# Kernel optimization log

Measured on AMD Instinct MI355X. Metric: run time of the kernel, lower is better.

The kernel has to match this reference:

```python
import jax, jax.numpy as jnp
import numpy as np

N_NODES = 50000
N_EDGES = 800000
IN_DIM = 128
HID = 128
N_GRAPHS = 256
N_CLASSES = 2
ALPHA = 0.2  # leaky relu slope
EPS_BN = 1e-5


def setup_inputs() -> dict:
    key = jax.random.key(0)
    ks = jax.random.split(key, 24)
    adjacency = jax.random.randint(ks[0], (2, N_EDGES), 0, N_NODES, dtype=jnp.int32)
    input_feature = jax.random.normal(ks[1], (N_NODES, IN_DIM), dtype=jnp.float32)
    graph_indicator = jnp.sort(jax.random.randint(ks[2], (N_NODES,), 0, N_GRAPHS, dtype=jnp.int32))
    labels = jax.random.randint(ks[3], (N_GRAPHS,), 0, N_CLASSES, dtype=jnp.int64)
    s = 0.05
    params = {
        'W1': jax.random.normal(ks[4], (IN_DIM, HID), jnp.float32) * s,
        'a1': jax.random.normal(ks[5], (2 * HID,), jnp.float32) * s,
        'bn2_g': jnp.ones((HID,), jnp.float32),
        'bn2_b': jnp.zeros((HID,), jnp.float32),
        'W2': jax.random.normal(ks[6], (HID, HID), jnp.float32) * s,
        'a2': jax.random.normal(ks[7], (2 * HID,), jnp.float32) * s,
        'bn3_g': jnp.ones((HID,), jnp.float32),
        'bn3_b': jnp.zeros((HID,), jnp.float32),
        'W3': jax.random.normal(ks[8], (HID, HID), jnp.float32) * s,
        'a3': jax.random.normal(ks[9], (2 * HID,), jnp.float32) * s,
        'fc1_w': jax.random.normal(ks[10], (HID, 2 * HID), jnp.float32) * s,
        'fc1_b': jnp.zeros((2 * HID,), jnp.float32),
        'fc2_w': jax.random.normal(ks[11], (2 * HID, HID), jnp.float32) * s,
        'fc2_b': jnp.zeros((HID,), jnp.float32),
        'fc3_w': jax.random.normal(ks[12], (HID, N_CLASSES), jnp.float32) * s,
        'fc3_b': jnp.zeros((N_CLASSES,), jnp.float32),
    }
    return dict(adjacency=adjacency, input_feature=input_feature,
                graph_indicator=graph_indicator, labels=labels, **params)


def _batchnorm(x, g, b):
    # training-mode BatchNorm1d over node dim (biased variance)
    mu = jnp.mean(x, axis=0)
    var = jnp.mean((x - mu) ** 2, axis=0)
    return (x - mu) * jax.lax.rsqrt(var + EPS_BN) * g + b


def _sp_gat(x, src, dst, W, a):
    # pyGAT SpGraphAttentionLayer (dropout disabled / eval mode)
    h = x @ W                                # [N, F]
    F = h.shape[1]
    e_src = h @ a[:F]                        # [N]
    e_dst = h @ a[F:]                        # [N]
    e = e_src[src] + e_dst[dst]              # [E]
    ee = jnp.exp(-jax.nn.leaky_relu(e, ALPHA))
    rowsum = jax.ops.segment_sum(ee, src, num_segments=N_NODES)          # [N]
    num = jax.ops.segment_sum(ee[:, None] * h[dst], src, num_segments=N_NODES)  # [N, F]
    h_prime = num / (rowsum[:, None] + 1e-16)
    return jax.nn.elu(h_prime)


def reference(adjacency, input_feature, graph_indicator, labels,
              W1, a1, bn2_g, bn2_b, W2, a2, bn3_g, bn3_b, W3, a3,
              fc1_w, fc1_b, fc2_w, fc2_b, fc3_w, fc3_b):
    src, dst = adjacency[0], adjacency[1]
    # bn1 output is discarded in the original forward
    x = _sp_gat(input_feature, src, dst, W1, a1)
    x = _batchnorm(x, bn2_g, bn2_b)
    x = _sp_gat(x, src, dst, W2, a2)
    x = _batchnorm(x, bn3_g, bn3_b)
    x = _sp_gat(x, src, dst, W3, a3)
    # pooling_sum_4tensor: per-graph sum pooling
    pooled = jax.ops.segment_sum(x, graph_indicator, num_segments=N_GRAPHS)  # [G, F]
    x = jax.nn.relu(pooled @ fc1_w + fc1_b)
    x = jax.nn.relu(x @ fc2_w + fc2_b)
    logits = x @ fc3_w + fc3_b
    return logits
```

## Files before the change

kernel.cpp:

```cpp
#include <hip/hip_runtime.h>
#include <hip/hip_bf16.h>

#define N_NODES 50000
#define N_EDGES 800000
#define FD 128
#define N_GRAPHS 256
#define NPART 6250

typedef unsigned short u16;
typedef short bf16x8 __attribute__((ext_vector_type(8)));
typedef float f32x4 __attribute__((ext_vector_type(4)));

__device__ __forceinline__ u16 f2bf(float v) {
    __hip_bfloat16 h = __float2bfloat16(v);
    union { __hip_bfloat16 hh; u16 u; } c; c.hh = h; return c.u;
}
__device__ __forceinline__ float bf2f(u16 r) {
    return __uint_as_float(((unsigned int)r) << 16);
}

__global__ __launch_bounds__(256) void count_deg_part_k(const int* __restrict__ src,
                                                        int* __restrict__ cnt, int E) {
    int part = blockIdx.x & 7;
    int lo = part * NPART, hi = lo + NPART;
    int stride = (gridDim.x >> 3) * 256;
    for (int e = (blockIdx.x >> 3) * 256 + threadIdx.x; e < E; e += stride) {
        int s = src[e];
        if (s >= lo && s < hi) atomicAdd(&cnt[s], 1);
    }
}

__global__ __launch_bounds__(256) void fill_csr_part_k(const int* __restrict__ src,
                                                       const int* __restrict__ dst,
                                                       int* __restrict__ cur,
                                                       int* __restrict__ edst, int E) {
    int part = blockIdx.x & 7;
    int lo = part * NPART, hi = lo + NPART;
    int stride = (gridDim.x >> 3) * 256;
    for (int e = (blockIdx.x >> 3) * 256 + threadIdx.x; e < E; e += stride) {
        int s = src[e];
        if (s >= lo && s < hi) {
            int p = atomicAdd(&cur[s], 1);
            edst[p] = dst[e];
        }
    }
}

__global__ __launch_bounds__(256) void scan1_k(const int* __restrict__ cnt,
                                               int* __restrict__ bsum, int M,
                                               float* __restrict__ bnbuf,
                                               float* __restrict__ pooled) {
    int i = blockIdx.x * 256 + threadIdx.x;
    int v = (i < M) ? cnt[i] : 0;
    __shared__ int l[256];
    l[threadIdx.x] = v;
    __syncthreads();
    for (int s = 128; s > 0; s >>= 1) {
        if (threadIdx.x < s) l[threadIdx.x] += l[threadIdx.x + s];
        __syncthreads();
    }
    if (threadIdx.x == 0) bsum[blockIdx.x] = l[0];
    if (blockIdx.x == 0) {
        bnbuf[threadIdx.x] = 0.f; bnbuf[threadIdx.x + 256] = 0.f;
        for (int k = threadIdx.x; k < N_GRAPHS * FD; k += 256) pooled[k] = 0.f;
    }
}

__global__ __launch_bounds__(256) void scan3_k(const int* __restrict__ cnt,
                                               const int* __restrict__ bsum,
                                               int* __restrict__ offs,
                                               int* __restrict__ cur, int M, int NB) {
    int i = blockIdx.x * 256 + threadIdx.x;
    int tid = threadIdx.x;
    __shared__ int bs[256];
    bs[tid] = (tid < NB) ? bsum[tid] : 0;
    __syncthreads();
    for (int off = 1; off < 256; off <<= 1) {
        int t = (tid >= off) ? bs[tid - off] : 0;
        __syncthreads();
        bs[tid] += t;
        __syncthreads();
    }
    int base = (blockIdx.x == 0) ? 0 : bs[blockIdx.x - 1];
    int v = (i < M) ? cnt[i] : 0;
    __shared__ int l[256];
    l[tid] = v;
    __syncthreads();
    for (int off = 1; off < 256; off <<= 1) {
        int t = (tid >= off) ? l[tid - off] : 0;
        __syncthreads();
        l[tid] += t;
        __syncthreads();
    }
    int excl = l[tid] - v + base;
    if (i < M) { offs[i] = excl; cur[i] = excl; }
    if (i == M - 1) offs[M] = excl + v;
}

__global__ __launch_bounds__(256) void gemm_mfma_k(const float* __restrict__ Xf,
                                                   const u16* __restrict__ Xb,
                                                   int use_f32,
                                                   const float* __restrict__ W,
                                                   const float* __restrict__ sums,
                                                   const float* __restrict__ sumsq,
                                                   const float* __restrict__ g,
                                                   const float* __restrict__ b,
                                                   float invN, int haveBN,
                                                   const float* __restrict__ avec,
                                                   u16* __restrict__ Hb,
                                                   float* __restrict__ es,
                                                   float* __restrict__ ed, int M) {
    __shared__ u16 As[64][136];
    __shared__ u16 Bs[128][136];
    __shared__ float cv[128];
    __shared__ float scsh[256];
    int tid = threadIdx.x;
    int row0 = blockIdx.x * 64;

    if (haveBN) {
        if (tid < 128) {
            float mu = sums[tid] * invN;
            float var = sumsq[tid] * invN - mu * mu;
            float sc = g[tid] * rsqrtf(var + 1e-5f);
            scsh[tid] = sc;
            scsh[128 + tid] = b[tid] - mu * sc;
        }
        __syncthreads();
        float cvp = 0.f;
#pragma unroll 8
        for (int i = 0; i < 64; i++) {
            int idx = i * 256 + tid;
            int k = idx >> 7;
            int n = idx & 127;
            float wv = W[idx];
            Bs[n][k] = f2bf(scsh[k] * wv);
            cvp += scsh[128 + k] * wv;
        }
        __syncthreads();
        scsh[tid] = cvp;
        __syncthreads();
        if (tid < 128) cv[tid] = scsh[tid] + scsh[tid + 128];
    } else {
#pragma unroll 8
        for (int i = 0; i < 64; i++) {
            int idx = i * 256 + tid;
            Bs[idx & 127][idx >> 7] = f2bf(W[idx]);
        }
        if (tid < 128) cv[tid] = 0.f;
    }

    {
        int r = tid >> 2, k0 = (tid & 3) * 32;
        int grow = row0 + r;
        if (grow < M) {
            if (use_f32) {
                const float4* s = (const float4*)(Xf + (size_t)grow * FD + k0);
#pragma unroll
                for (int u = 0; u < 8; u++) {
                    float4 v = s[u];
                    ushort4 o;
                    o.x = f2bf(v.x); o.y = f2bf(v.y); o.z = f2bf(v.z); o.w = f2bf(v.w);
                    *(ushort4*)&As[r][k0 + u * 4] = o;
                }
            } else {
                const uint4* s = (const uint4*)(Xb + (size_t)grow * FD + k0);
#pragma unroll
                for (int u = 0; u < 4; u++) *(uint4*)&As[r][k0 + u * 8] = s[u];
            }
        } else {
            uint4 z = make_uint4(0, 0, 0, 0);
#pragma unroll
            for (int u = 0; u < 4; u++) *(uint4*)&As[r][k0 + u * 8] = z;
        }
    }
    __syncthreads();

    int wave = tid >> 6, lane = tid & 63;
    int quad = lane >> 4, n16 = lane & 15;
    int rbase = wave * 16;
    f32x4 acc[8];
    f32x4 zz = {0.f, 0.f, 0.f, 0.f};
#pragma unroll
    for (int t = 0; t < 8; t++) acc[t] = zz;

#pragma unroll
    for (int kk = 0; kk < 128; kk += 32) {
        bf16x8 a = *(const bf16x8*)&As[rbase + n16][kk + quad * 8];
#pragma unroll
        for (int t = 0; t < 8; t++) {
            bf16x8 bb = *(const bf16x8*)&Bs[t * 16 + n16][kk + quad * 8];
            acc[t] = __builtin_amdgcn_mfma_f32_16x16x32_bf16(a, bb, acc[t], 0, 0, 0);
        }
    }

    float sas[8], sad[8];
#pragma unroll
    for (int t = 0; t < 8; t++) {
        sas[t] = avec[t * 16 + n16];
        sad[t] = avec[128 + t * 16 + n16];
    }

#pragma unroll
    for (int reg = 0; reg < 4; reg++) {
        int grow = row0 + rbase + quad * 4 + reg;
        float vals[8];
        float ps = 0.f, pd = 0.f;
#pragma unroll
        for (int t = 0; t < 8; t++) {
            float v = acc[t][reg] + cv[t * 16 + n16];
            vals[t] = v;
            ps += v * sas[t];
            pd += v * sad[t];
        }
#pragma unroll
        for (int o = 8; o > 0; o >>= 1) { ps += __shfl_xor(ps, o); pd += __shfl_xor(pd, o); }
        if (grow < M) {
            if (n16 == 0) { es[grow] = ps; ed[grow] = pd; }
#pragma unroll
            for (int t = 0; t < 8; t++)
                Hb[(size_t)grow * FD + t * 16 + n16] = f2bf(vals[t]);
        }
    }
}

__global__ __launch_bounds__(256) void agg_k(const u16* __restrict__ Hb,
                                             const float* __restrict__ es_,
                                             const float* __restrict__ ed_,
                                             const int* __restrict__ offs,
                                             const int* __restrict__ edst,
                                             u16* __restrict__ Out, int M) {
    int node = __builtin_amdgcn_readfirstlane((int)((blockIdx.x * blockDim.x + threadIdx.x) >> 6));
    int lane = threadIdx.x & 63;
    if (node >= M) return;
    int s0 = offs[node], s1 = offs[node + 1];
    float esv = es_[node];
    const unsigned int* Hrow = (const unsigned int*)Hb;
    float2 a0 = make_float2(0.f, 0.f), a1 = make_float2(0.f, 0.f);
    float2 a2 = make_float2(0.f, 0.f), a3 = make_float2(0.f, 0.f);
    float rs = 0.f;
    int e = s0;
    for (; e + 8 <= s1; e += 8) {
        int d0 = __builtin_amdgcn_readfirstlane(edst[e]);
        int d1 = __builtin_amdgcn_readfirstlane(edst[e + 1]);
        int d2 = __builtin_amdgcn_readfirstlane(edst[e + 2]);
        int d3 = __builtin_amdgcn_readfirstlane(edst[e + 3]);
        int d4 = __builtin_amdgcn_readfirstlane(edst[e + 4]);
        int d5 = __builtin_amdgcn_readfirstlane(edst[e + 5]);
        int d6 = __builtin_amdgcn_readfirstlane(edst[e + 6]);
        int d7 = __builtin_amdgcn_readfirstlane(edst[e + 7]);
        float w0, w1, w2, w3, w4, w5, w6, w7;
        {
            float ev = esv + ed_[d0]; float lr = ev > 0.f ? ev : 0.2f * ev; w0 = __expf(-lr);
        }
        { float ev = esv + ed_[d1]; float lr = ev > 0.f ? ev : 0.2f * ev; w1 = __expf(-lr); }
        { float ev = esv + ed_[d2]; float lr = ev > 0.f ? ev : 0.2f * ev; w2 = __expf(-lr); }
        { float ev = esv + ed_[d3]; float lr = ev > 0.f ? ev : 0.2f * ev; w3 = __expf(-lr); }
        { float ev = esv + ed_[d4]; float lr = ev > 0.f ? ev : 0.2f * ev; w4 = __expf(-lr); }
        { float ev = esv + ed_[d5]; float lr = ev > 0.f ? ev : 0.2f * ev; w5 = __expf(-lr); }
        { float ev = esv + ed_[d6]; float lr = ev > 0.f ? ev : 0.2f * ev; w6 = __expf(-lr); }
        { float ev = esv + ed_[d7]; float lr = ev > 0.f ? ev : 0.2f * ev; w7 = __expf(-lr); }
        unsigned int r0 = Hrow[(size_t)d0 * 64 + lane];
        unsigned int r1 = Hrow[(size_t)d1 * 64 + lane];
        unsigned int r2 = Hrow[(size_t)d2 * 64 + lane];
        unsigned int r3 = Hrow[(size_t)d3 * 64 + lane];
        unsigned int r4 = Hrow[(size_t)d4 * 64 + lane];
        unsigned int r5 = Hrow[(size_t)d5 * 64 + lane];
        unsigned int r6 = Hrow[(size_t)d6 * 64 + lane];
        unsigned int r7 = Hrow[(size_t)d7 * 64 + lane];
        rs += w0 + w1 + w2 + w3 + w4 + w5 + w6 + w7;
        a0.x += w0 * __uint_as_float(r0 << 16);
        a0.y += w0 * __uint_as_float(r0 & 0xffff0000u);
        a1.x += w1 * __uint_as_float(r1 << 16);
        a1.y += w1 * __uint_as_float(r1 & 0xffff0000u);
        a2.x += w2 * __uint_as_float(r2 << 16);
        a2.y += w2 * __uint_as_float(r2 & 0xffff0000u);
        a3.x += w3 * __uint_as_float(r3 << 16);
        a3.y += w3 * __uint_as_float(r3 & 0xffff0000u);
        a0.x += w4 * __uint_as_float(r4 << 16);
        a0.y += w4 * __uint_as_float(r4 & 0xffff0000u);
        a1.x += w5 * __uint_as_float(r5 << 16);
        a1.y += w5 * __uint_as_float(r5 & 0xffff0000u);
        a2.x += w6 * __uint_as_float(r6 << 16);
        a2.y += w6 * __uint_as_float(r6 & 0xffff0000u);
        a3.x += w7 * __uint_as_float(r7 << 16);
        a3.y += w7 * __uint_as_float(r7 & 0xffff0000u);
    }
    for (; e < s1; e++) {
        int d = __builtin_amdgcn_readfirstlane(edst[e]);
        float ev = esv + ed_[d];
        float lr = ev > 0.f ? ev : 0.2f * ev;
        float wv = __expf(-lr);
        rs += wv;
        unsigned int r = Hrow[(size_t)d * 64 + lane];
        a0.x += wv * __uint_as_float(r << 16);
        a0.y += wv * __uint_as_float(r & 0xffff0000u);
    }
    float inv = 1.f / (rs + 1e-16f);
    float vx = (a0.x + a1.x + a2.x + a3.x) * inv;
    float vy = (a0.y + a1.y + a2.y + a3.y) * inv;
    vx = vx > 0.f ? vx : (__expf(vx) - 1.f);
    vy = vy > 0.f ? vy : (__expf(vy) - 1.f);
    unsigned int pk = ((unsigned int)f2bf(vy) << 16) | f2bf(vx);
    ((unsigned int*)Out)[(size_t)node * 64 + lane] = pk;
}

__global__ void bnstats_b_k(const u16* __restrict__ Xb, float* __restrict__ sums,
                            float* __restrict__ sumsq, int M) {
    int f = threadIdx.x & 127;
    int half = threadIdx.x >> 7;
    float s1 = 0.f, s2 = 0.f;
    for (int r = blockIdx.x * 2 + half; r < M; r += gridDim.x * 2) {
        float v = bf2f(Xb[(size_t)r * FD + f]);
        s1 += v; s2 += v * v;
    }
    __shared__ float l1[256], l2[256];
    l1[threadIdx.x] = s1; l2[threadIdx.x] = s2;
    __syncthreads();
    if (half == 0) {
        atomicAdd(&sums[f], l1[f] + l1[f + 128]);
        atomicAdd(&sumsq[f], l2[f] + l2[f + 128]);
    }
}

__global__ void pool_k(const u16* __restrict__ Xb, const int* __restrict__ gi,
                       float* __restrict__ pooled, int M) {
    int f = threadIdx.x & 127;
    int half = threadIdx.x >> 7;
    int r0 = blockIdx.x * 128 + half;
    int rend = min(blockIdx.x * 128 + 128, M);
    int curg = -1; float acc = 0.f;
    for (int r = r0; r < rend; r += 2) {
        int g = gi[r];
        if (g != curg) {
            if (curg >= 0) atomicAdd(&pooled[(size_t)curg * FD + f], acc);
            curg = g; acc = 0.f;
        }
        acc += bf2f(Xb[(size_t)r * FD + f]);
    }
    if (curg >= 0) atomicAdd(&pooled[(size_t)curg * FD + f], acc);
}

__global__ __launch_bounds__(256) void mlp_k(const float* __restrict__ pooled,
                                             const float* __restrict__ fc1w, const float* __restrict__ fc1b,
                                             const float* __restrict__ fc2w, const float* __restrict__ fc2b,
                                             const float* __restrict__ fc3w, const float* __restrict__ fc3b,
                                             float* __restrict__ out) {
    int g = blockIdx.x, j = threadIdx.x;
    __shared__ float x[128], t1[256], t2[128], p0[128], p1[128];
    if (j < 128) x[j] = pooled[(size_t)g * FD + j];
    __syncthreads();
    float s = fc1b[j];
    for (int k = 0; k < 128; k++) s += x[k] * fc1w[(size_t)k * 256 + j];
    t1[j] = fmaxf(s, 0.f);
    __syncthreads();
    if (j < 128) {
        float s2 = fc2b[j];
        for (int k = 0; k < 256; k++) s2 += t1[k] * fc2w[(size_t)k * 128 + j];
        t2[j] = fmaxf(s2, 0.f);
    }
    __syncthreads();
    if (j < 128) { p0[j] = t2[j] * fc3w[j * 2]; p1[j] = t2[j] * fc3w[j * 2 + 1]; }
    __syncthreads();
    for (int s3 = 64; s3 > 0; s3 >>= 1) {
        if (j < s3) { p0[j] += p0[j + s3]; p1[j] += p1[j + s3]; }
        __syncthreads();
    }
    if (j == 0) { out[g * 2] = p0[0] + fc3b[0]; out[g * 2 + 1] = p1[0] + fc3b[1]; }
}

extern "C" void kernel_launch(void* const* d_in, const int* in_sizes, int n_in,
                              void* d_out, int out_size, void* d_ws, size_t ws_size,
                              hipStream_t stream) {
    const int*   adj  = (const int*)d_in[0];
    const float* xin  = (const float*)d_in[1];
    const int*   gi   = (const int*)d_in[2];
    const float* W1   = (const float*)d_in[4];
    const float* a1   = (const float*)d_in[5];
    const float* bn2g = (const float*)d_in[6];
    const float* bn2b = (const float*)d_in[7];
    const float* W2   = (const float*)d_in[8];
    const float* a2   = (const float*)d_in[9];
    const float* bn3g = (const float*)d_in[10];
    const float* bn3b = (const float*)d_in[11];
    const float* W3   = (const float*)d_in[12];
    const float* a3   = (const float*)d_in[13];
    const float* fc1w = (const float*)d_in[14];
    const float* fc1b = (const float*)d_in[15];
    const float* fc2w = (const float*)d_in[16];
    const float* fc2b = (const float*)d_in[17];
    const float* fc3w = (const float*)d_in[18];
    const float* fc3b = (const float*)d_in[19];
    float* out = (float*)d_out;

    const int N = N_NODES, E = N_EDGES, G = N_GRAPHS;

    u16*   Xb     = (u16*)d_ws;
    u16*   Hb     = Xb + (size_t)N * FD;
    u16*   Wt     = Hb + (size_t)N * FD;
    float* es     = (float*)(Wt + FD * FD);
    float* ed     = es + N;
    float* bnbuf  = ed + N;
    float* sumsA  = bnbuf;
    float* sumsqA = bnbuf + 128;
    float* sumsB  = bnbuf + 256;
    float* sumsqB = bnbuf + 384;
    float* cvec   = bnbuf + 512;
    float* pooled = cvec + FD;
    int*   degcnt = (int*)(pooled + (size_t)G * FD);
    int*   offs   = degcnt + N;
    int*   cur    = offs + (N + 2);
    int*   bsum   = cur + N;
    int*   edst   = bsum + 256;

    const int* srcp = adj;
    const int* dstp = adj + E;

    const int NB = (N + 255) / 256;

    hipMemsetAsync(degcnt, 0, (size_t)N * sizeof(int), stream);
    count_deg_part_k<<<8 * 392, 256, 0, stream>>>(srcp, degcnt, E);
    scan1_k<<<NB, 256, 0, stream>>>(degcnt, bsum, N, bnbuf, pooled);
    scan3_k<<<NB, 256, 0, stream>>>(degcnt, bsum, offs, cur, N, NB);
    fill_csr_part_k<<<8 * 392, 256, 0, stream>>>(srcp, dstp, cur, edst, E);

    const int gemm_grid = (N + 63) / 64;
    const int wave_grid = (N + 3) / 4;
    const float invN = 1.0f / (float)N;

    gemm_mfma_k<<<gemm_grid, 256, 0, stream>>>(xin, Xb, 1, W1,
                                               nullptr, nullptr, nullptr, nullptr, invN, 0,
                                               a1, Hb, es, ed, N);
    agg_k<<<wave_grid, 256, 0, stream>>>(Hb, es, ed, offs, edst, Xb, N);
    bnstats_b_k<<<256, 256, 0, stream>>>(Xb, sumsA, sumsqA, N);

    gemm_mfma_k<<<gemm_grid, 256, 0, stream>>>(nullptr, Xb, 0, W2,
                                               sumsA, sumsqA, bn2g, bn2b, invN, 1,
                                               a2, Hb, es, ed, N);
    agg_k<<<wave_grid, 256, 0, stream>>>(Hb, es, ed, offs, edst, Xb, N);
    bnstats_b_k<<<256, 256, 0, stream>>>(Xb, sumsB, sumsqB, N);

    gemm_mfma_k<<<gemm_grid, 256, 0, stream>>>(nullptr, Xb, 0, W3,
                                               sumsB, sumsqB, bn3g, bn3b, invN, 1,
                                               a3, Hb, es, ed, N);
    agg_k<<<wave_grid, 256, 0, stream>>>(Hb, es, ed, offs, edst, Xb, N);

    pool_k<<<(N + 127) / 128, 256, 0, stream>>>(Xb, gi, pooled, N);
    mlp_k<<<G, 256, 0, stream>>>(pooled, fc1w, fc1b, fc2w, fc2b, fc3w, fc3b, out);
}
```

Before: 425.8 us.

## Split wavefront into four edge groups with 16-byte row gathers in GAT aggregation

The aggregation kernel now splits each 64-lane wavefront into four 16-lane groups. Each group handles a different edge and loads a full bf16 row with 16-byte vector loads, so a wavefront processes 8 edges per iteration in two rounds. Partial sums are reduced across groups with xor shuffles, and one group writes the output row. This aims to raise memory-level parallelism and use wider loads instead of serial 4-byte gathers per edge. In exchange it adds shuffle reductions, clamped and masked tail edges that do wasted work, and per-lane divergent index loads instead of scalar ones.

```diff
diff --git a/kernel.cpp b/kernel.cpp
--- a/kernel.cpp
+++ b/kernel.cpp
@@ -234,74 +234,64 @@
     if (node >= M) return;
     int s0 = offs[node], s1 = offs[node + 1];
     float esv = es_[node];
-    const unsigned int* Hrow = (const unsigned int*)Hb;
-    float2 a0 = make_float2(0.f, 0.f), a1 = make_float2(0.f, 0.f);
-    float2 a2 = make_float2(0.f, 0.f), a3 = make_float2(0.f, 0.f);
-    float rs = 0.f;
-    int e = s0;
-    for (; e + 8 <= s1; e += 8) {
-        int d0 = __builtin_amdgcn_readfirstlane(edst[e]);
-        int d1 = __builtin_amdgcn_readfirstlane(edst[e + 1]);
-        int d2 = __builtin_amdgcn_readfirstlane(edst[e + 2]);
-        int d3 = __builtin_amdgcn_readfirstlane(edst[e + 3]);
-        int d4 = __builtin_amdgcn_readfirstlane(edst[e + 4]);
-        int d5 = __builtin_amdgcn_readfirstlane(edst[e + 5]);
-        int d6 = __builtin_amdgcn_readfirstlane(edst[e + 6]);
-        int d7 = __builtin_amdgcn_readfirstlane(edst[e + 7]);
-        float w0, w1, w2, w3, w4, w5, w6, w7;
-        {
-            float ev = esv + ed_[d0]; float lr = ev > 0.f ? ev : 0.2f * ev; w0 = __expf(-lr);
-        }
-        { float ev = esv + ed_[d1]; float lr = ev > 0.f ? ev : 0.2f * ev; w1 = __expf(-lr); }
-        { float ev = esv + ed_[d2]; float lr = ev > 0.f ? ev : 0.2f * ev; w2 = __expf(-lr); }
-        { float ev = esv + ed_[d3]; float lr = ev > 0.f ? ev : 0.2f * ev; w3 = __expf(-lr); }
-        { float ev = esv + ed_[d4]; float lr = ev > 0.f ? ev : 0.2f * ev; w4 = __expf(-lr); }
-        { float ev = esv + ed_[d5]; float lr = ev > 0.f ? ev : 0.2f * ev; w5 = __expf(-lr); }
-        { float ev = esv + ed_[d6]; float lr = ev > 0.f ? ev : 0.2f * ev; w6 = __expf(-lr); }
-        { float ev = esv + ed_[d7]; float lr = ev > 0.f ? ev : 0.2f * ev; w7 = __expf(-lr); }
-        unsigned int r0 = Hrow[(size_t)d0 * 64 + lane];
-        unsigned int r1 = Hrow[(size_t)d1 * 64 + lane];
-        unsigned int r2 = Hrow[(size_t)d2 * 64 + lane];
-        unsigned int r3 = Hrow[(size_t)d3 * 64 + lane];
-        unsigned int r4 = Hrow[(size_t)d4 * 64 + lane];
-        unsigned int r5 = Hrow[(size_t)d5 * 64 + lane];
-        unsigned int r6 = Hrow[(size_t)d6 * 64 + lane];
-        unsigned int r7 = Hrow[(size_t)d7 * 64 + lane];
-        rs += w0 + w1 + w2 + w3 + w4 + w5 + w6 + w7;
-        a0.x += w0 * __uint_as_float(r0 << 16);
-        a0.y += w0 * __uint_as_float(r0 & 0xffff0000u);
-        a1.x += w1 * __uint_as_float(r1 << 16);
-        a1.y += w1 * __uint_as_float(r1 & 0xffff0000u);
-        a2.x += w2 * __uint_as_float(r2 << 16);
-        a2.y += w2 * __uint_as_float(r2 & 0xffff0000u);
-        a3.x += w3 * __uint_as_float(r3 << 16);
-        a3.y += w3 * __uint_as_float(r3 & 0xffff0000u);
-        a0.x += w4 * __uint_as_float(r4 << 16);
-        a0.y += w4 * __uint_as_float(r4 & 0xffff0000u);
-        a1.x += w5 * __uint_as_float(r5 << 16);
-        a1.y += w5 * __uint_as_float(r5 & 0xffff0000u);
-        a2.x += w6 * __uint_as_float(r6 << 16);
-        a2.y += w6 * __uint_as_float(r6 & 0xffff0000u);
-        a3.x += w7 * __uint_as_float(r7 << 16);
-        a3.y += w7 * __uint_as_float(r7 & 0xffff0000u);
-    }
-    for (; e < s1; e++) {
-        int d = __builtin_amdgcn_readfirstlane(edst[e]);
-        float ev = esv + ed_[d];
-        float lr = ev > 0.f ? ev : 0.2f * ev;
-        float wv = __expf(-lr);
-        rs += wv;
-        unsigned int r = Hrow[(size_t)d * 64 + lane];
-        a0.x += wv * __uint_as_float(r << 16);
-        a0.y += wv * __uint_as_float(r & 0xffff0000u);
+    int q = lane >> 4;
+    int f16 = lane & 15;
+    const uint4* Hq = (const uint4*)Hb;
+    float acc[8];
+#pragma unroll
+    for (int j = 0; j < 8; j++) acc[j] = 0.f;
+    float rsl = 0.f;
+    int last = s1 - 1;
+    for (int e = s0; e < s1; e += 8) {
+        int eA = e + q;
+        int eB = e + 4 + q;
+        int iA = eA <= last ? eA : last;
+        int iB = eB <= last ? eB : last;
+        int dA = edst[iA];
+        int dB = edst[iB];
+        float evA = esv + ed_[dA];
+        float evB = esv + ed_[dB];
+        uint4 rA = Hq[(size_t)dA * 16 + f16];
+        uint4 rB = Hq[(size_t)dB * 16 + f16];
+        float lrA = evA > 0.f ? evA : 0.2f * evA;
+        float lrB = evB > 0.f ? evB : 0.2f * evB;
+        float wA = __expf(-lrA);
+        float wB = __expf(-lrB);
+        if (eA > last) wA = 0.f;
+        if (eB > last) wB = 0.f;
+        rsl += wA + wB;
+        unsigned int ra[4] = {rA.x, rA.y, rA.z, rA.w};
+        unsigned int rb[4] = {rB.x, rB.y, rB.z, rB.w};
+#pragma unroll
+        for (int k = 0; k < 4; k++) {
+            acc[2 * k]     += wA * __uint_as_float(ra[k] << 16)
+                            + wB * __uint_as_float(rb[k] << 16);
+            acc[2 * k + 1] += wA * __uint_as_float(ra[k] & 0xffff0000u)
+                            + wB * __uint_as_float(rb[k] & 0xffff0000u);
+        }
+    }
+    float rs = rsl;
+    rs += __shfl_xor(rs, 16);
+    rs += __shfl_xor(rs, 32);
+#pragma unroll
+    for (int j = 0; j < 8; j++) {
+        acc[j] += __shfl_xor(acc[j], 16);
+        acc[j] += __shfl_xor(acc[j], 32);
     }
     float inv = 1.f / (rs + 1e-16f);
-    float vx = (a0.x + a1.x + a2.x + a3.x) * inv;
-    float vy = (a0.y + a1.y + a2.y + a3.y) * inv;
-    vx = vx > 0.f ? vx : (__expf(vx) - 1.f);
-    vy = vy > 0.f ? vy : (__expf(vy) - 1.f);
-    unsigned int pk = ((unsigned int)f2bf(vy) << 16) | f2bf(vx);
-    ((unsigned int*)Out)[(size_t)node * 64 + lane] = pk;
+    unsigned int pk[4];
+#pragma unroll
+    for (int k = 0; k < 4; k++) {
+        float v0 = acc[2 * k] * inv;
+        float v1 = acc[2 * k + 1] * inv;
+        v0 = v0 > 0.f ? v0 : (__expf(v0) - 1.f);
+        v1 = v1 > 0.f ? v1 : (__expf(v1) - 1.f);
+        pk[k] = ((unsigned int)f2bf(v1) << 16) | f2bf(v0);
+    }
+    if (q == 0) {
+        uint4 o = make_uint4(pk[0], pk[1], pk[2], pk[3]);
+        ((uint4*)(Out + (size_t)node * FD))[f16] = o;
+    }
 }
 
 __global__ void bnstats_b_k(const u16* __restrict__ Xb, float* __restrict__ sums,
```

Result: no change. 420.1 us (-1.3%).
